# Kernel optimization log

Hardware: AMD Instinct MI355X
Metric: run time of the kernel (lower is better)

The kernel has to match this reference:

```python
import jax, jax.numpy as jnp
import numpy as np

GROUPS = 32
HEADS = 8
EPS = 1e-5


def setup_inputs() -> dict:
    key = jax.random.key(0)
    ks = jax.random.split(key, 3)
    b, c, h, w = 8, 512, 32, 32
    x = jax.random.normal(ks[0], (b, c, h, w), dtype=jnp.float32)
    gn_w = jnp.ones((c,), jnp.float32)
    gn_b = jnp.zeros((c,), jnp.float32)
    qkv_w = jax.random.normal(ks[1], (3 * c, c), dtype=jnp.float32) * (1.0 / np.sqrt(c))
    qkv_b = jnp.zeros((3 * c,), jnp.float32)
    proj_w = jax.random.normal(ks[2], (c, c), dtype=jnp.float32) * (1.0 / np.sqrt(c))
    proj_b = jnp.zeros((c,), jnp.float32)
    return {"x": x, "gn_w": gn_w, "gn_b": gn_b, "qkv_w": qkv_w,
            "qkv_b": qkv_b, "proj_w": proj_w, "proj_b": proj_b}


def group_norm(x, weight, bias):
    b, c, h, w = x.shape
    xg = x.reshape(b, GROUPS, c // GROUPS, h, w)
    mean = xg.mean(axis=(2, 3, 4), keepdims=True)
    var = xg.var(axis=(2, 3, 4), keepdims=True)
    xn = ((xg - mean) * jax.lax.rsqrt(var + EPS)).reshape(b, c, h, w)
    return xn * weight[None, :, None, None] + bias[None, :, None, None]


def reference(x, gn_w, gn_b, qkv_w, qkv_b, proj_w, proj_b):
    b, c, h, w = x.shape
    dh = c // HEADS
    xn = group_norm(x, gn_w, gn_b)
    # 1x1 conv == per-pixel linear: (b,c,h,w) x (3c,c) -> (b,3c,h,w)
    qkv = jnp.einsum('bchw,oc->bohw', xn, qkv_w) + qkv_b[None, :, None, None]
    qkv = qkv.reshape(b, 3, HEADS, dh, h * w)  # 'three' outermost, then heads, head_dim
    q, k, v = qkv[:, 0], qkv[:, 1], qkv[:, 2]  # (b, heads, dh, hw)
    scale = dh ** (-0.5)
    attn = jax.nn.softmax(jnp.einsum('bhci,bhcj->bhij', q, k) * scale, axis=-1)
    out = jnp.einsum('bhij,bhcj->bhci', attn, v)  # (b, heads, dh, hw)
    out = out.reshape(b, c, h, w)
    out = jnp.einsum('bchw,oc->bohw', out, proj_w) + proj_b[None, :, None, None]
    return x + out
```

## Files before the change

kernel.cpp:

```cpp
#include <hip/hip_runtime.h>
#include <cstdint>
#include <cstddef>

#define BATCH 8
#define CCH   512
#define SSP   1024
#define NH    8
#define DH    64
#define O3    1536

typedef __bf16 bf16x8 __attribute__((ext_vector_type(8)));
typedef float  f32x4  __attribute__((ext_vector_type(4)));

__device__ __forceinline__ unsigned short f2bf(float f) {
    unsigned u = __builtin_bit_cast(unsigned, f);
    unsigned r = u + 0x7fffu + ((u >> 16) & 1u);
    return (unsigned short)(r >> 16);
}

__device__ __forceinline__ unsigned pk2bf(float lo, float hi) {
    unsigned ul = __builtin_bit_cast(unsigned, lo) + 0x8000u;
    unsigned uh = __builtin_bit_cast(unsigned, hi) + 0x8000u;
    return __builtin_amdgcn_perm(uh, ul, 0x07060302u);
}

__device__ __forceinline__ bf16x8 ld8(const unsigned short* p) {
    uint4 u = *(const uint4*)p;
    return __builtin_bit_cast(bf16x8, u);
}

__device__ __forceinline__ void glls16(const void* g, void* l) {
    __builtin_amdgcn_global_load_lds(
        (const __attribute__((address_space(1))) unsigned*)g,
        (__attribute__((address_space(3))) unsigned*)l, 16, 0, 0);
}

__global__ __launch_bounds__(256) void gn_wconv(const float* __restrict__ x,
                                                const float* __restrict__ gw,
                                                const float* __restrict__ gb,
                                                unsigned short* __restrict__ xnt,
                                                const float* __restrict__ s1,
                                                unsigned short* __restrict__ d1, int n1,
                                                const float* __restrict__ s2,
                                                unsigned short* __restrict__ d2) {
    int t = threadIdx.x;
    if (blockIdx.x >= 256) {
        int i = (blockIdx.x - 256) * 256 + t;
        const float4* sp;
        ushort4* dp;
        if (i < n1) { sp = (const float4*)s1 + i; dp = (ushort4*)d1 + i; }
        else        { sp = (const float4*)s2 + (i - n1); dp = (ushort4*)d2 + (i - n1); }
        float4 v = *sp;
        ushort4 o;
        o.x = f2bf(v.x); o.y = f2bf(v.y); o.z = f2bf(v.z); o.w = f2bf(v.w);
        *dp = o;
        return;
    }

    int blk = blockIdx.x;
    int b = blk >> 5, g = blk & 31;
    const float4* xp = (const float4*)(x + (size_t)(b * CCH + g * 16) * SSP);

    float4 vals[16];
    float sum = 0.f, ss = 0.f;
#pragma unroll
    for (int i = 0; i < 16; i++) {
        float4 v = xp[i * 256 + t];
        vals[i] = v;
        sum += (v.x + v.y) + (v.z + v.w);
        ss  += (v.x * v.x + v.y * v.y) + (v.z * v.z + v.w * v.w);
    }
#pragma unroll
    for (int o = 32; o; o >>= 1) {
        sum += __shfl_xor(sum, o, 64);
        ss  += __shfl_xor(ss,  o, 64);
    }
    __shared__ float red[8];
    if ((t & 63) == 0) { red[(t >> 6) * 2] = sum; red[(t >> 6) * 2 + 1] = ss; }
    __syncthreads();
    sum = red[0] + red[2] + red[4] + red[6];
    ss  = red[1] + red[3] + red[5] + red[7];

    float mean = sum * (1.f / 16384.f);
    float var  = ss * (1.f / 16384.f) - mean * mean;
    float rstd = rsqrtf(var + 1e-5f);

    __shared__ unsigned short tile[16][1032];
#pragma unroll
    for (int i = 0; i < 16; i++) {
        int f4 = i * 256 + t;
        int c = f4 >> 8;
        int s = (f4 & 255) * 4;
        float wsc = gw[g * 16 + c] * rstd;
        float bia = gb[g * 16 + c] - mean * wsc;
        float4 v = vals[i];
        tile[c][s + 0] = f2bf(v.x * wsc + bia);
        tile[c][s + 1] = f2bf(v.y * wsc + bia);
        tile[c][s + 2] = f2bf(v.z * wsc + bia);
        tile[c][s + 3] = f2bf(v.w * wsc + bia);
    }
    __syncthreads();

    int c2 = (t & 7) * 2, sr = t >> 3;
    unsigned short* outbase = xnt + (size_t)b * SSP * CCH + g * 16 + c2;
#pragma unroll
    for (int i = 0; i < 32; i++) {
        int s = i * 32 + sr;
        unsigned v = (unsigned)tile[c2][s] | ((unsigned)tile[c2 + 1][s] << 16);
        *(unsigned*)(outbase + (size_t)s * CCH) = v;
    }
}

__global__ __launch_bounds__(256) void gemm_qkv(const unsigned short* __restrict__ Aall,
                                                const unsigned short* __restrict__ Bw,
                                                const float* __restrict__ bias,
                                                unsigned short* __restrict__ Call,
                                                unsigned short* __restrict__ vtout) {
    const int K = 512;
    int bz = blockIdx.z;
    const unsigned short* A = Aall + (size_t)bz * SSP * CCH;
    int m0 = blockIdx.x * 128, n0 = blockIdx.y * 128;

    __shared__ unsigned short As[128 * 64], Bs[128 * 64];
    int t = threadIdx.x, wave = t >> 6, lane = t & 63;
    int quad = lane >> 4, l16 = lane & 15;
    int wm = (wave & 1) * 64, wn = (wave >> 1) * 64;

    int lrow = lane >> 3;
    int lc   = ((lane & 7) - lrow) & 7;
    const unsigned short* Ag = A  + (size_t)(m0 + wave * 32 + lrow) * K + lc * 8;
    const unsigned short* Bg = Bw + (size_t)(n0 + wave * 32 + lrow) * K + lc * 8;
    unsigned short* Asw = As + wave * 2048;
    unsigned short* Bsw = Bs + wave * 2048;

    f32x4 acc[4][4];
#pragma unroll
    for (int i = 0; i < 4; i++)
#pragma unroll
        for (int j = 0; j < 4; j++) acc[i][j] = f32x4{0.f, 0.f, 0.f, 0.f};

    int rowA = (wm + l16) * 64, rowB = (wn + l16) * 64;
    int cph[2];
#pragma unroll
    for (int kc = 0; kc < 2; kc++) cph[kc] = ((quad + 4 * kc + l16) & 7) * 8;

    for (int k0 = 0; k0 < K; k0 += 64) {
        __syncthreads();
#pragma unroll
        for (int i = 0; i < 4; i++) {
            glls16(Ag + (size_t)i * 8 * K + k0, Asw + i * 512);
            glls16(Bg + (size_t)i * 8 * K + k0, Bsw + i * 512);
        }
        __syncthreads();
#pragma unroll
        for (int kc = 0; kc < 2; kc++) {
            bf16x8 af[4], bfr[4];
#pragma unroll
            for (int i = 0; i < 4; i++) {
                af[i]  = ld8(As + rowA + i * 1024 + cph[kc]);
                bfr[i] = ld8(Bs + rowB + i * 1024 + cph[kc]);
            }
#pragma unroll
            for (int i = 0; i < 4; i++)
#pragma unroll
                for (int j = 0; j < 4; j++)
                    acc[i][j] = __builtin_amdgcn_mfma_f32_16x16x32_bf16(af[i], bfr[j], acc[i][j], 0, 0, 0);
        }
    }

    if (n0 < 1024) {
        unsigned short* Cp = Call + (size_t)bz * SSP * O3;
#pragma unroll
        for (int i = 0; i < 4; i++)
#pragma unroll
            for (int j = 0; j < 4; j++) {
                int col = n0 + wn + j * 16 + l16;
                float bv = bias[col];
#pragma unroll
                for (int r = 0; r < 4; r++) {
                    int row = m0 + wm + i * 16 + quad * 4 + r;
                    Cp[(size_t)row * O3 + col] = f2bf(acc[i][j][r] + bv);
                }
            }
    } else {
#pragma unroll
        for (int j = 0; j < 4; j++) {
            int col = n0 + wn + j * 16 + l16;
            float bv = bias[col];
            unsigned short* vp = vtout + ((size_t)bz * 512 + (col - 1024)) * SSP;
#pragma unroll
            for (int i = 0; i < 4; i++) {
                int s = m0 + wm + i * 16 + quad * 4;
                uint2 d;
                d.x = pk2bf(acc[i][j][0] + bv, acc[i][j][1] + bv);
                d.y = pk2bf(acc[i][j][2] + bv, acc[i][j][3] + bv);
                *(uint2*)(vp + s) = d;
            }
        }
    }
}

__global__ __launch_bounds__(256) void gemm_proj(const unsigned short* __restrict__ Pw,
                                                 const unsigned short* __restrict__ Oall,
                                                 const float* __restrict__ bias,
                                                 const float* __restrict__ xres,
                                                 float* __restrict__ Out) {
    const int K = 512;
    int bz = blockIdx.z;
    const unsigned short* Bv = Oall + (size_t)bz * SSP * CCH;
    int m0 = blockIdx.x * 64, n0 = blockIdx.y * 128;

    __shared__ unsigned short As[64 * 64], Bs[128 * 64];
    int t = threadIdx.x, wave = t >> 6, lane = t & 63;
    int quad = lane >> 4, l16 = lane & 15;
    int wr = (wave & 1) * 32, wc = (wave >> 1) * 64;

    int lrow = lane >> 3;
    int lc   = ((lane & 7) - lrow) & 7;
    const unsigned short* Ag = Pw + (size_t)(m0 + wave * 16 + lrow) * K + lc * 8;
    const unsigned short* Bg = Bv + (size_t)(n0 + wave * 32 + lrow) * K + lc * 8;
    unsigned short* Asw = As + wave * 1024;
    unsigned short* Bsw = Bs + wave * 2048;

    f32x4 acc[2][4];
#pragma unroll
    for (int i = 0; i < 2; i++)
#pragma unroll
        for (int j = 0; j < 4; j++) acc[i][j] = f32x4{0.f, 0.f, 0.f, 0.f};

    int rowA = (wr + l16) * 64, rowB = (wc + l16) * 64;
    int cph[2];
#pragma unroll
    for (int kc = 0; kc < 2; kc++) cph[kc] = ((quad + 4 * kc + l16) & 7) * 8;

    for (int k0 = 0; k0 < K; k0 += 64) {
        __syncthreads();
#pragma unroll
        for (int i = 0; i < 2; i++)
            glls16(Ag + (size_t)i * 8 * K + k0, Asw + i * 512);
#pragma unroll
        for (int i = 0; i < 4; i++)
            glls16(Bg + (size_t)i * 8 * K + k0, Bsw + i * 512);
        __syncthreads();
#pragma unroll
        for (int kc = 0; kc < 2; kc++) {
            bf16x8 af[2], bfr[4];
#pragma unroll
            for (int i = 0; i < 2; i++) af[i]  = ld8(As + rowA + i * 1024 + cph[kc]);
#pragma unroll
            for (int j = 0; j < 4; j++) bfr[j] = ld8(Bs + rowB + j * 1024 + cph[kc]);
#pragma unroll
            for (int i = 0; i < 2; i++)
#pragma unroll
                for (int j = 0; j < 4; j++)
                    acc[i][j] = __builtin_amdgcn_mfma_f32_16x16x32_bf16(af[i], bfr[j], acc[i][j], 0, 0, 0);
        }
    }
#pragma unroll
    for (int i = 0; i < 2; i++)
#pragma unroll
        for (int j = 0; j < 4; j++) {
            int col = n0 + wc + j * 16 + l16;
#pragma unroll
            for (int r = 0; r < 4; r++) {
                int row = m0 + wr + i * 16 + quad * 4 + r;
                size_t idx = (size_t)bz * CCH * SSP + (size_t)row * SSP + col;
                Out[idx] = xres[idx] + acc[i][j][r] + bias[row];
            }
        }
}

__global__ __launch_bounds__(256, 4) void attn(const unsigned short* __restrict__ qkvt,
                                               const unsigned short* __restrict__ vt,
                                               unsigned short* __restrict__ ot) {
    int blk = blockIdx.x;
    int xcd = blk & 7, jj = blk >> 3;
    int bh = xcd * 8 + (jj >> 4);
    int i0 = (jj & 15) * 64;
    int b = bh >> 3, h = bh & 7;

    __shared__ unsigned short Ks[128][72];
    __shared__ unsigned short Vs[64][136];

    int t = threadIdx.x, wave = t >> 6, lane = t & 63;
    int quad = lane >> 4, l16 = lane & 15;
    const float c1 = 0.125f * 1.44269504f;

    unsigned short* Ps = &Ks[0][0] + wave * (16 * 136);

    bf16x8 qf[2];
    {
        const unsigned short* qp =
            qkvt + ((size_t)b * SSP + i0 + wave * 16 + l16) * O3 + h * DH + quad * 8;
        qf[0] = ld8(qp);
        qf[1] = ld8(qp + 32);
    }

    f32x4 Oa[4];
#pragma unroll
    for (int i = 0; i < 4; i++) Oa[i] = f32x4{0.f, 0.f, 0.f, 0.f};
    float m_run = -INFINITY, l_run = 0.f;

    int jr = t >> 3, c8 = (t & 7) * 8;
    int cr = t >> 4, j8 = (t & 15) * 8;

    for (int jb = 0; jb < 8; jb++) {
        int j0 = jb * 128;
        __syncthreads();
#pragma unroll
        for (int p = 0; p < 4; p++) {
            int row = p * 32 + jr;
            *(uint4*)&Ks[row][c8] =
                *(const uint4*)(qkvt + ((size_t)b * SSP + j0 + row) * O3 + CCH + h * DH + c8);
        }
#pragma unroll
        for (int p = 0; p < 4; p++) {
            *(uint4*)&Vs[p * 16 + cr][j8] =
                *(const uint4*)(vt + ((size_t)bh * DH + p * 16 + cr) * SSP + j0 + j8);
        }
        __syncthreads();

        f32x4 sc[8];
#pragma unroll
        for (int tj = 0; tj < 8; tj++) sc[tj] = f32x4{0.f, 0.f, 0.f, 0.f};
#pragma unroll
        for (int kc = 0; kc < 2; kc++)
#pragma unroll
            for (int tj = 0; tj < 8; tj++) {
                bf16x8 kf = ld8(&Ks[tj * 16 + l16][kc * 32 + quad * 8]);
                sc[tj] = __builtin_amdgcn_mfma_f32_16x16x32_bf16(kf, qf[kc], sc[tj], 0, 0, 0);
            }

        float m = sc[0][0];
#pragma unroll
        for (int tj = 0; tj < 8; tj++)
#pragma unroll
            for (int r = 0; r < 4; r++) m = fmaxf(m, sc[tj][r]);
        m = fmaxf(m, __shfl_xor(m, 16, 64));
        m = fmaxf(m, __shfl_xor(m, 32, 64));
        float mn = fmaxf(m_run, m);
        float alpha = __builtin_amdgcn_exp2f(c1 * (m_run - mn));
        m_run = mn;
        float cm = c1 * mn;
        float rs = 0.f;
#pragma unroll
        for (int tj = 0; tj < 8; tj++)
#pragma unroll
            for (int r = 0; r < 4; r++) {
                float p = __builtin_amdgcn_exp2f(c1 * sc[tj][r] - cm);
                sc[tj][r] = p;
                rs += p;
            }
        rs += __shfl_xor(rs, 16, 64);
        rs += __shfl_xor(rs, 32, 64);
        l_run = l_run * alpha + rs;

        __syncthreads();

#pragma unroll
        for (int tj = 0; tj < 8; tj++) {
            uint2 d;
            d.x = pk2bf(sc[tj][0], sc[tj][1]);
            d.y = pk2bf(sc[tj][2], sc[tj][3]);
            *(uint2*)&Ps[l16 * 136 + tj * 16 + quad * 4] = d;
        }

#pragma unroll
        for (int tc = 0; tc < 4; tc++)
#pragma unroll
            for (int r = 0; r < 4; r++) Oa[tc][r] *= alpha;
#pragma unroll
        for (int kj = 0; kj < 4; kj++) {
            bf16x8 pf = ld8(&Ps[l16 * 136 + kj * 32 + quad * 8]);
#pragma unroll
            for (int tc = 0; tc < 4; tc++) {
                bf16x8 vf = ld8(&Vs[tc * 16 + l16][kj * 32 + quad * 8]);
                Oa[tc] = __builtin_amdgcn_mfma_f32_16x16x32_bf16(vf, pf, Oa[tc], 0, 0, 0);
            }
        }
    }

    float rl = 1.f / l_run;
    int i = i0 + wave * 16 + l16;
    unsigned short* ob = ot + ((size_t)b * SSP + i) * CCH + h * DH;
#pragma unroll
    for (int tc = 0; tc < 4; tc++) {
        uint2 d;
        d.x = pk2bf(Oa[tc][0] * rl, Oa[tc][1] * rl);
        d.y = pk2bf(Oa[tc][2] * rl, Oa[tc][3] * rl);
        *(uint2*)(ob + tc * 16 + quad * 4) = d;
    }
}

extern "C" void kernel_launch(void* const* d_in, const int* in_sizes, int n_in,
                              void* d_out, int out_size, void* d_ws, size_t ws_size,
                              hipStream_t stream) {
    const float* x      = (const float*)d_in[0];
    const float* gn_w   = (const float*)d_in[1];
    const float* gn_b   = (const float*)d_in[2];
    const float* qkv_w  = (const float*)d_in[3];
    const float* qkv_b  = (const float*)d_in[4];
    const float* proj_w = (const float*)d_in[5];
    const float* proj_b = (const float*)d_in[6];
    float* out = (float*)d_out;

    char* ws = (char*)d_ws;
    unsigned short* xnt   = (unsigned short*)(ws);
    unsigned short* qw_bf = (unsigned short*)(ws + 8388608);
    unsigned short* pw_bf = (unsigned short*)(ws + 9961472);
    unsigned short* qkvt  = (unsigned short*)(ws + 10485760);
    unsigned short* vt    = (unsigned short*)(ws + 35651584);
    unsigned short* otb   = (unsigned short*)(ws + 44040192);

    gn_wconv<<<dim3(1280), dim3(256), 0, stream>>>(x, gn_w, gn_b, xnt,
                                                   qkv_w, qw_bf, 196608, proj_w, pw_bf);
    gemm_qkv<<<dim3(8, 12, 8), dim3(256), 0, stream>>>(xnt, qw_bf, qkv_b, qkvt, vt);
    attn<<<dim3(1024), dim3(256), 0, stream>>>(qkvt, vt, otb);
    gemm_proj<<<dim3(8, 8, 8), dim3(256), 0, stream>>>(pw_bf, otb, proj_b, x, out);
}
```

Baseline: 163.2 us.

## Process two query tiles per attention block to reuse K/V loads

```diff
diff --git a/kernel.cpp b/kernel.cpp
--- a/kernel.cpp
+++ b/kernel.cpp
@@ -270,36 +270,41 @@
         }
 }
 
-__global__ __launch_bounds__(256, 4) void attn(const unsigned short* __restrict__ qkvt,
+__global__ __launch_bounds__(256, 2) void attn(const unsigned short* __restrict__ qkvt,
                                                const unsigned short* __restrict__ vt,
                                                unsigned short* __restrict__ ot) {
     int blk = blockIdx.x;
     int xcd = blk & 7, jj = blk >> 3;
-    int bh = xcd * 8 + (jj >> 4);
-    int i0 = (jj & 15) * 64;
+    int bh = xcd * 8 + (jj >> 3);
+    int i0 = (jj & 7) * 128;
     int b = bh >> 3, h = bh & 7;
 
     __shared__ unsigned short Ks[128][72];
     __shared__ unsigned short Vs[64][136];
+    __shared__ unsigned short Ps1buf[4][16 * 136];
 
     int t = threadIdx.x, wave = t >> 6, lane = t & 63;
     int quad = lane >> 4, l16 = lane & 15;
     const float c1 = 0.125f * 1.44269504f;
 
-    unsigned short* Ps = &Ks[0][0] + wave * (16 * 136);
-
-    bf16x8 qf[2];
-    {
+    unsigned short* Ps0 = &Ks[0][0] + wave * (16 * 136);
+    unsigned short* Ps1 = &Ps1buf[wave][0];
+
+    bf16x8 qf[2][2];
+#pragma unroll
+    for (int hf = 0; hf < 2; hf++) {
         const unsigned short* qp =
-            qkvt + ((size_t)b * SSP + i0 + wave * 16 + l16) * O3 + h * DH + quad * 8;
-        qf[0] = ld8(qp);
-        qf[1] = ld8(qp + 32);
-    }
-
-    f32x4 Oa[4];
-#pragma unroll
-    for (int i = 0; i < 4; i++) Oa[i] = f32x4{0.f, 0.f, 0.f, 0.f};
-    float m_run = -INFINITY, l_run = 0.f;
+            qkvt + ((size_t)b * SSP + i0 + hf * 64 + wave * 16 + l16) * O3 + h * DH + quad * 8;
+        qf[0][hf] = ld8(qp);
+        qf[1][hf] = ld8(qp + 32);
+    }
+
+    f32x4 Oa[2][4];
+#pragma unroll
+    for (int hf = 0; hf < 2; hf++)
+#pragma unroll
+        for (int i = 0; i < 4; i++) Oa[hf][i] = f32x4{0.f, 0.f, 0.f, 0.f};
+    float m_run[2] = {-INFINITY, -INFINITY}, l_run[2] = {0.f, 0.f};
 
     int jr = t >> 3, c8 = (t & 7) * 8;
     int cr = t >> 4, j8 = (t & 15) * 8;
@@ -320,75 +325,92 @@
         }
         __syncthreads();
 
-        f32x4 sc[8];
-#pragma unroll
-        for (int tj = 0; tj < 8; tj++) sc[tj] = f32x4{0.f, 0.f, 0.f, 0.f};
+        f32x4 sc[2][8];
+#pragma unroll
+        for (int hf = 0; hf < 2; hf++)
+#pragma unroll
+            for (int tj = 0; tj < 8; tj++) sc[hf][tj] = f32x4{0.f, 0.f, 0.f, 0.f};
 #pragma unroll
         for (int kc = 0; kc < 2; kc++)
 #pragma unroll
             for (int tj = 0; tj < 8; tj++) {
                 bf16x8 kf = ld8(&Ks[tj * 16 + l16][kc * 32 + quad * 8]);
-                sc[tj] = __builtin_amdgcn_mfma_f32_16x16x32_bf16(kf, qf[kc], sc[tj], 0, 0, 0);
-            }
-
-        float m = sc[0][0];
-#pragma unroll
-        for (int tj = 0; tj < 8; tj++)
-#pragma unroll
-            for (int r = 0; r < 4; r++) m = fmaxf(m, sc[tj][r]);
-        m = fmaxf(m, __shfl_xor(m, 16, 64));
-        m = fmaxf(m, __shfl_xor(m, 32, 64));
-        float mn = fmaxf(m_run, m);
-        float alpha = __builtin_amdgcn_exp2f(c1 * (m_run - mn));
-        m_run = mn;
-        float cm = c1 * mn;
-        float rs = 0.f;
-#pragma unroll
-        for (int tj = 0; tj < 8; tj++)
-#pragma unroll
-            for (int r = 0; r < 4; r++) {
-                float p = __builtin_amdgcn_exp2f(c1 * sc[tj][r] - cm);
-                sc[tj][r] = p;
-                rs += p;
-            }
-        rs += __shfl_xor(rs, 16, 64);
-        rs += __shfl_xor(rs, 32, 64);
-        l_run = l_run * alpha + rs;
+                sc[0][tj] = __builtin_amdgcn_mfma_f32_16x16x32_bf16(kf, qf[kc][0], sc[0][tj], 0, 0, 0);
+                sc[1][tj] = __builtin_amdgcn_mfma_f32_16x16x32_bf16(kf, qf[kc][1], sc[1][tj], 0, 0, 0);
+            }
+
+        float alpha[2];
+#pragma unroll
+        for (int hf = 0; hf < 2; hf++) {
+            float m = sc[hf][0][0];
+#pragma unroll
+            for (int tj = 0; tj < 8; tj++)
+#pragma unroll
+                for (int r = 0; r < 4; r++) m = fmaxf(m, sc[hf][tj][r]);
+            m = fmaxf(m, __shfl_xor(m, 16, 64));
+            m = fmaxf(m, __shfl_xor(m, 32, 64));
+            float mn = fmaxf(m_run[hf], m);
+            alpha[hf] = __builtin_amdgcn_exp2f(c1 * (m_run[hf] - mn));
+            m_run[hf] = mn;
+            float cm = c1 * mn;
+            float rs = 0.f;
+#pragma unroll
+            for (int tj = 0; tj < 8; tj++)
+#pragma unroll
+                for (int r = 0; r < 4; r++) {
+                    float p = __builtin_amdgcn_exp2f(c1 * sc[hf][tj][r] - cm);
+                    sc[hf][tj][r] = p;
+                    rs += p;
+                }
+            rs += __shfl_xor(rs, 16, 64);
+            rs += __shfl_xor(rs, 32, 64);
+            l_run[hf] = l_run[hf] * alpha[hf] + rs;
+        }
 
         __syncthreads();
 
 #pragma unroll
         for (int tj = 0; tj < 8; tj++) {
-            uint2 d;
-            d.x = pk2bf(sc[tj][0], sc[tj][1]);
-            d.y = pk2bf(sc[tj][2], sc[tj][3]);
-            *(uint2*)&Ps[l16 * 136 + tj * 16 + quad * 4] = d;
-        }
-
-#pragma unroll
-        for (int tc = 0; tc < 4; tc++)
-#pragma unroll
-            for (int r = 0; r < 4; r++) Oa[tc][r] *= alpha;
+            uint2 d0, d1;
+            d0.x = pk2bf(sc[0][tj][0], sc[0][tj][1]);
+            d0.y = pk2bf(sc[0][tj][2], sc[0][tj][3]);
+            d1.x = pk2bf(sc[1][tj][0], sc[1][tj][1]);
+            d1.y = pk2bf(sc[1][tj][2], sc[1][tj][3]);
+            *(uint2*)&Ps0[l16 * 136 + tj * 16 + quad * 4] = d0;
+            *(uint2*)&Ps1[l16 * 136 + tj * 16 + quad * 4] = d1;
+        }
+
+#pragma unroll
+        for (int hf = 0; hf < 2; hf++)
+#pragma unroll
+            for (int tc = 0; tc < 4; tc++)
+#pragma unroll
+                for (int r = 0; r < 4; r++) Oa[hf][tc][r] *= alpha[hf];
 #pragma unroll
         for (int kj = 0; kj < 4; kj++) {
-            bf16x8 pf = ld8(&Ps[l16 * 136 + kj * 32 + quad * 8]);
+            bf16x8 pf0 = ld8(&Ps0[l16 * 136 + kj * 32 + quad * 8]);
+            bf16x8 pf1 = ld8(&Ps1[l16 * 136 + kj * 32 + quad * 8]);
 #pragma unroll
             for (int tc = 0; tc < 4; tc++) {
                 bf16x8 vf = ld8(&Vs[tc * 16 + l16][kj * 32 + quad * 8]);
-                Oa[tc] = __builtin_amdgcn_mfma_f32_16x16x32_bf16(vf, pf, Oa[tc], 0, 0, 0);
-            }
-        }
-    }
-
-    float rl = 1.f / l_run;
-    int i = i0 + wave * 16 + l16;
-    unsigned short* ob = ot + ((size_t)b * SSP + i) * CCH + h * DH;
-#pragma unroll
-    for (int tc = 0; tc < 4; tc++) {
-        uint2 d;
-        d.x = pk2bf(Oa[tc][0] * rl, Oa[tc][1] * rl);
-        d.y = pk2bf(Oa[tc][2] * rl, Oa[tc][3] * rl);
-        *(uint2*)(ob + tc * 16 + quad * 4) = d;
+                Oa[0][tc] = __builtin_amdgcn_mfma_f32_16x16x32_bf16(vf, pf0, Oa[0][tc], 0, 0, 0);
+                Oa[1][tc] = __builtin_amdgcn_mfma_f32_16x16x32_bf16(vf, pf1, Oa[1][tc], 0, 0, 0);
+            }
+        }
+    }
+
+#pragma unroll
+    for (int hf = 0; hf < 2; hf++) {
+        float rl = 1.f / l_run[hf];
+        int i = i0 + hf * 64 + wave * 16 + l16;
+        unsigned short* ob = ot + ((size_t)b * SSP + i) * CCH + h * DH;
+#pragma unroll
+        for (int tc = 0; tc < 4; tc++) {
+            uint2 d;
+            d.x = pk2bf(Oa[hf][tc][0] * rl, Oa[hf][tc][1] * rl);
+            d.y = pk2bf(Oa[hf][tc][2] * rl, Oa[hf][tc][3] * rl);
+            *(uint2*)(ob + tc * 16 + quad * 4) = d;
+        }
     }
 }
 
@@ -415,6 +437,6 @@
     gn_wconv<<<dim3(1280), dim3(256), 0, stream>>>(x, gn_w, gn_b, xnt,
                                                    qkv_w, qw_bf, 196608, proj_w, pw_bf);
     gemm_qkv<<<dim3(8, 12, 8), dim3(256), 0, stream>>>(xnt, qw_bf, qkv_b, qkvt, vt);
-    attn<<<dim3(1024), dim3(256), 0, stream>>>(qkvt, vt, otb);
+    attn<<<dim3(512), dim3(256), 0, stream>>>(qkvt, vt, otb);
     gemm_proj<<<dim3(8, 8, 8), dim3(256), 0, stream>>>(pw_bf, otb, proj_b, x, out);
 }
```

Result: slower. 169.6 us (+3.9%).

## Double-buffer K/V tiles in attention with async global-to-LDS loads and swizzled layout

Applied to the files above, without the earlier changes.

```diff
diff --git a/kernel.cpp b/kernel.cpp
--- a/kernel.cpp
+++ b/kernel.cpp
@@ -270,7 +270,7 @@
         }
 }
 
-__global__ __launch_bounds__(256, 4) void attn(const unsigned short* __restrict__ qkvt,
+__global__ __launch_bounds__(256, 2) void attn(const unsigned short* __restrict__ qkvt,
                                                const unsigned short* __restrict__ vt,
                                                unsigned short* __restrict__ ot) {
     int blk = blockIdx.x;
@@ -279,14 +279,15 @@
     int i0 = (jj & 15) * 64;
     int b = bh >> 3, h = bh & 7;
 
-    __shared__ unsigned short Ks[128][72];
-    __shared__ unsigned short Vs[64][136];
+    __shared__ unsigned short KsD[2][128 * 64];
+    __shared__ unsigned short VsD[2][64 * 128];
+    __shared__ unsigned short PsD[4][16 * 128];
 
     int t = threadIdx.x, wave = t >> 6, lane = t & 63;
     int quad = lane >> 4, l16 = lane & 15;
     const float c1 = 0.125f * 1.44269504f;
 
-    unsigned short* Ps = &Ks[0][0] + wave * (16 * 136);
+    unsigned short* Ps = PsD[wave];
 
     bf16x8 qf[2];
     {
@@ -301,24 +302,44 @@
     for (int i = 0; i < 4; i++) Oa[i] = f32x4{0.f, 0.f, 0.f, 0.f};
     float m_run = -INFINITY, l_run = 0.f;
 
-    int jr = t >> 3, c8 = (t & 7) * 8;
-    int cr = t >> 4, j8 = (t & 15) * 8;
+    int lrow8 = lane >> 3, lc8 = ((lane & 7) - lrow8) & 7;
+    const unsigned short* kga = qkvt + (size_t)b * SSP * O3 + CCH + h * DH;
+    size_t koff[4];
+    int klds[4];
+#pragma unroll
+    for (int p = 0; p < 4; p++) {
+        koff[p] = (size_t)(wave * 32 + p * 8 + lrow8) * O3 + lc8 * 8;
+        klds[p] = (wave * 32 + p * 8) * 64;
+    }
+    int lrow16 = lane >> 4;
+    const unsigned short* vga = vt + (size_t)bh * DH * SSP;
+    int voff[4], vlds[4];
+#pragma unroll
+    for (int p = 0; p < 4; p++) {
+        int lcv = ((lane & 15) - p * 4 - lrow16) & 15;
+        voff[p] = (wave * 16 + p * 4 + lrow16) * SSP + lcv * 8;
+        vlds[p] = (wave * 16 + p * 4) * 128;
+    }
+
+#pragma unroll
+    for (int p = 0; p < 4; p++) glls16(kga + koff[p], &KsD[0][klds[p]]);
+#pragma unroll
+    for (int p = 0; p < 4; p++) glls16(vga + voff[p], &VsD[0][vlds[p]]);
+    __syncthreads();
 
     for (int jb = 0; jb < 8; jb++) {
-        int j0 = jb * 128;
-        __syncthreads();
-#pragma unroll
-        for (int p = 0; p < 4; p++) {
-            int row = p * 32 + jr;
-            *(uint4*)&Ks[row][c8] =
-                *(const uint4*)(qkvt + ((size_t)b * SSP + j0 + row) * O3 + CCH + h * DH + c8);
-        }
-#pragma unroll
-        for (int p = 0; p < 4; p++) {
-            *(uint4*)&Vs[p * 16 + cr][j8] =
-                *(const uint4*)(vt + ((size_t)bh * DH + p * 16 + cr) * SSP + j0 + j8);
-        }
-        __syncthreads();
+        int cur = jb & 1;
+        if (jb < 7) {
+            int nxt = cur ^ 1;
+            size_t j1k = (size_t)(jb + 1) * 128 * O3;
+            int j1v = (jb + 1) * 128;
+#pragma unroll
+            for (int p = 0; p < 4; p++) glls16(kga + j1k + koff[p], &KsD[nxt][klds[p]]);
+#pragma unroll
+            for (int p = 0; p < 4; p++) glls16(vga + j1v + voff[p], &VsD[nxt][vlds[p]]);
+        }
+        const unsigned short* ks = KsD[cur];
+        const unsigned short* vs = VsD[cur];
 
         f32x4 sc[8];
 #pragma unroll
@@ -327,7 +348,8 @@
         for (int kc = 0; kc < 2; kc++)
 #pragma unroll
             for (int tj = 0; tj < 8; tj++) {
-                bf16x8 kf = ld8(&Ks[tj * 16 + l16][kc * 32 + quad * 8]);
+                int krow = tj * 16 + l16;
+                bf16x8 kf = ld8(ks + krow * 64 + ((kc * 4 + quad + l16) & 7) * 8);
                 sc[tj] = __builtin_amdgcn_mfma_f32_16x16x32_bf16(kf, qf[kc], sc[tj], 0, 0, 0);
             }
 
@@ -355,14 +377,13 @@
         rs += __shfl_xor(rs, 32, 64);
         l_run = l_run * alpha + rs;
 
-        __syncthreads();
-
 #pragma unroll
         for (int tj = 0; tj < 8; tj++) {
             uint2 d;
             d.x = pk2bf(sc[tj][0], sc[tj][1]);
             d.y = pk2bf(sc[tj][2], sc[tj][3]);
-            *(uint2*)&Ps[l16 * 136 + tj * 16 + quad * 4] = d;
+            int pc = (tj * 2 + (quad >> 1) + l16) & 15;
+            *(uint2*)(Ps + l16 * 128 + pc * 8 + (quad & 1) * 4) = d;
         }
 
 #pragma unroll
@@ -371,13 +392,16 @@
             for (int r = 0; r < 4; r++) Oa[tc][r] *= alpha;
 #pragma unroll
         for (int kj = 0; kj < 4; kj++) {
-            bf16x8 pf = ld8(&Ps[l16 * 136 + kj * 32 + quad * 8]);
+            int pch = (kj * 4 + quad + l16) & 15;
+            bf16x8 pf = ld8(Ps + l16 * 128 + pch * 8);
 #pragma unroll
             for (int tc = 0; tc < 4; tc++) {
-                bf16x8 vf = ld8(&Vs[tc * 16 + l16][kj * 32 + quad * 8]);
+                bf16x8 vf = ld8(vs + (tc * 16 + l16) * 128 + ((kj * 4 + quad + l16) & 15) * 8);
                 Oa[tc] = __builtin_amdgcn_mfma_f32_16x16x32_bf16(vf, pf, Oa[tc], 0, 0, 0);
             }
         }
+
+        __syncthreads();
     }
 
     float rl = 1.f / l_run;
```

Result: no change. 163.9 us (+0.4%).
